# Optimization experiments

Hardware: AMD Instinct MI355X
Metric: run time of the kernel (lower is better)

## Reference

```python
import jax, jax.numpy as jnp
import numpy as np

B, S, D_IN, E, H = 4, 2048, 768, 768, 12
HD = E // H                      # 64
WIN_PCT = 10                     # window_size init arg (percent of valid length)
MAX_LEN = 2048
MIN_WIN = 2
PAD = -1e9
TEMP = 1.0


def setup_inputs() -> dict:
    key = jax.random.key(0)
    k1, k2, k3 = jax.random.split(key, 3)
    return {
        "x": jax.random.normal(k1, (B, S, D_IN), dtype=jnp.float32),
        "src_key_padding_mask": jnp.zeros((B, S), dtype=jnp.int32),   # 0 = valid token
        "matrix_mask": jnp.zeros((B, S, S), dtype=jnp.float32),       # additive mask, 0 or PAD
        "qkv_w": jax.random.normal(k2, (3 * E, D_IN), dtype=jnp.float32) * 0.02,
        "qkv_b": jnp.zeros((3 * E,), dtype=jnp.float32),
        "o_w": jax.random.normal(k3, (E, E), dtype=jnp.float32) * 0.02,
        "o_b": jnp.zeros((E,), dtype=jnp.float32),
    }


def _sliding_window_mask(src_key_padding_mask, matrix_mask):
    # per-sample window size = ceil(valid_len * WIN_PCT / 100), clamped to >= MIN_WIN
    lens = (src_key_padding_mask == 0).sum(axis=1)                    # [B]
    clipped = jnp.minimum(lens, MAX_LEN).astype(jnp.float32)
    wsz = jnp.maximum(jnp.ceil(clipped * WIN_PCT / 100.0), MIN_WIN)   # [B] float ok for compare
    idx = jnp.arange(S)
    dist = jnp.abs(idx[None, :, None] - idx[None, None, :])           # [1,S,S]
    window_mask = dist > wsz[:, None, None]                           # [B,S,S] bool
    merged = window_mask | (matrix_mask == PAD)
    return jnp.where(merged, PAD, matrix_mask)                        # [B,S,S]


def reference(x, src_key_padding_mask, matrix_mask, qkv_w, qkv_b, o_w, o_b):
    mask = _sliding_window_mask(src_key_padding_mask, matrix_mask)    # [B,S,S]
    qkv = x @ qkv_w.T + qkv_b                                         # [B,S,3E]
    # torch: reshape(B,S,H,3*HD) then chunk along last dim
    qkv = qkv.reshape(B, S, H, 3 * HD).transpose(0, 2, 1, 3)          # [B,H,S,3*HD]
    q, k, v = jnp.split(qkv, 3, axis=-1)                              # each [B,H,S,HD]
    scale = 1.0 / np.sqrt(HD)
    logits = jnp.einsum("bhqd,bhkd->bhqk", q, k) * scale + mask[:, None]
    attn = jax.nn.softmax(logits / TEMP, axis=-1)                     # [B,H,S,S]
    values = jnp.einsum("bhqk,bhkd->bhqd", attn, v)                   # [B,H,S,HD]
    attn_mean = attn.mean(axis=1)                                     # [B,S,S]
    values = values.transpose(0, 2, 1, 3).reshape(B, S, E)            # [B,S,E]
    o = values @ o_w.T + o_b
    return (o, attn_mean)
```

## Files before the change

kernel.cpp:

```cpp
#include <hip/hip_runtime.h>

#define SEQ 2048
#define NB 4
#define DIN 768
#define EDIM 768
#define NH 12
#define QKVN 2304
#define SCALE 0.125f
#define PADV -1e9f
#define INV12 (0.0833333333f)
#define PSW 520

typedef unsigned short ushort_t;
typedef __attribute__((ext_vector_type(8))) short bf16x8;
typedef __attribute__((ext_vector_type(4))) float f32x4;

__device__ __forceinline__ float bf2f(ushort_t u) {
    union { unsigned int i; float f; } v; v.i = ((unsigned int)u) << 16; return v.f;
}
__device__ __forceinline__ ushort_t f2bf(float f) {
    union { float f; unsigned int i; } v; v.f = f;
    unsigned int r = (v.i + 0x7fffu + ((v.i >> 16) & 1u)) >> 16;
    return (ushort_t)r;
}
__device__ __forceinline__ void gl_lds16(const ushort_t* g, ushort_t* l) {
    __builtin_amdgcn_global_load_lds(
        (const __attribute__((address_space(1))) unsigned int*)(g),
        (__attribute__((address_space(3))) unsigned int*)(l),
        16, 0, 0);
}

__global__ void cvt3_kernel(const float* __restrict__ s0, int n0,
                            const float* __restrict__ s1, int n1,
                            const float* __restrict__ s2, int n2,
                            ushort_t* __restrict__ d0, ushort_t* __restrict__ d1,
                            ushort_t* __restrict__ d2) {
    int i = blockIdx.x * blockDim.x + threadIdx.x;
    const float* src; ushort_t* dst; int off;
    if (i < n0)               { src = s0; dst = d0; off = i; }
    else if (i < n0 + n1)     { src = s1; dst = d1; off = i - n0; }
    else if (i < n0 + n1 + n2){ src = s2; dst = d2; off = i - n0 - n1; }
    else return;
    float4 f = ((const float4*)src)[off];
    ushort4 u;
    u.x = f2bf(f.x); u.y = f2bf(f.y); u.z = f2bf(f.z); u.w = f2bf(f.w);
    ((ushort4*)dst)[off] = u;
}

template<int MODE>
__global__ __launch_bounds__(256) void mfma_gemm128(
    const ushort_t* __restrict__ A, const ushort_t* __restrict__ Bw,
    const float* __restrict__ bias, float* __restrict__ outf,
    ushort_t* __restrict__ qkh, ushort_t* __restrict__ vt, int N, int K)
{
    __shared__ __align__(16) ushort_t Al[128 * 64];
    __shared__ __align__(16) ushort_t Bl[128 * 64];
    const int tid  = threadIdx.x;
    const int w    = tid >> 6;
    const int l    = tid & 63;
    const int quad = l >> 4;
    const int lr   = l & 15;
    const int mw   = (w >> 1) * 64;
    const int nw   = (w & 1) * 64;
    const int bm   = blockIdx.y * 128;
    const int bn   = blockIdx.x * 128;
    const int srow = l >> 3;
    const int sg   = (l & 7) ^ srow;

    f32x4 acc[4][4];
    #pragma unroll
    for (int i = 0; i < 4; ++i)
        #pragma unroll
        for (int j = 0; j < 4; ++j)
            #pragma unroll
            for (int r = 0; r < 4; ++r) acc[i][j][r] = 0.f;

    const ushort_t* ga = A  + (size_t)(bm + w * 32 + srow) * K + sg * 8;
    const ushort_t* gb = Bw + (size_t)(bn + w * 32 + srow) * K + sg * 8;
    ushort_t* la = &Al[(w * 32) * 64];
    ushort_t* lb = &Bl[(w * 32) * 64];

    for (int k0 = 0; k0 < K; k0 += 64) {
        __syncthreads();
        #pragma unroll
        for (int i = 0; i < 4; ++i)
            gl_lds16(ga + (size_t)(i * 8) * K + k0, la + i * 8 * 64);
        #pragma unroll
        for (int i = 0; i < 4; ++i)
            gl_lds16(gb + (size_t)(i * 8) * K + k0, lb + i * 8 * 64);
        __syncthreads();
        #pragma unroll
        for (int s = 0; s < 2; ++s) {
            bf16x8 af[4], bf[4];
            #pragma unroll
            for (int t = 0; t < 4; ++t)
                af[t] = *(const bf16x8*)&Al[(mw + t * 16 + lr) * 64 + (((4 * s + quad) ^ (lr & 7)) * 8)];
            #pragma unroll
            for (int t = 0; t < 4; ++t)
                bf[t] = *(const bf16x8*)&Bl[(nw + t * 16 + lr) * 64 + (((4 * s + quad) ^ (lr & 7)) * 8)];
            #pragma unroll
            for (int mt = 0; mt < 4; ++mt)
                #pragma unroll
                for (int nt = 0; nt < 4; ++nt)
                    acc[mt][nt] = __builtin_amdgcn_mfma_f32_16x16x32_bf16(af[mt], bf[nt], acc[mt][nt], 0, 0, 0);
        }
    }

    #pragma unroll
    for (int nt = 0; nt < 4; ++nt) {
        const int gn = bn + nw + nt * 16 + lr;
        const float bv = bias[gn];
        const int hh  = gn / 192;
        const int rem = gn - hh * 192;
        #pragma unroll
        for (int mt = 0; mt < 4; ++mt) {
            const int gm0 = bm + mw + mt * 16 + quad * 4;
            if (MODE == 0) {
                #pragma unroll
                for (int r = 0; r < 4; ++r)
                    outf[(size_t)(gm0 + r) * N + gn] = acc[mt][nt][r] + bv;
            } else if (rem < 128) {
                const int bb  = gm0 >> 11;
                const int tok = gm0 & (SEQ - 1);
                #pragma unroll
                for (int r = 0; r < 4; ++r)
                    qkh[((size_t)(bb * NH + hh) * SEQ + tok + r) * 128 + rem] =
                        f2bf(acc[mt][nt][r] + bv);
            } else {
                const int bb  = gm0 >> 11;
                const int tok = gm0 & (SEQ - 1);
                ushort4 st;
                st.x = f2bf(acc[mt][nt][0] + bv);
                st.y = f2bf(acc[mt][nt][1] + bv);
                st.z = f2bf(acc[mt][nt][2] + bv);
                st.w = f2bf(acc[mt][nt][3] + bv);
                *(ushort4*)&vt[((size_t)(bb * NH + hh) * 64 + (rem - 128)) * SEQ + tok] = st;
            }
        }
    }
}

__global__ __launch_bounds__(512) void attn_kernel(
    const ushort_t* __restrict__ qkh,
    const ushort_t* __restrict__ vt,
    const float* __restrict__ mmask,
    const int* __restrict__ pad,
    ushort_t* __restrict__ values,
    float* __restrict__ attn_out)
{
    __shared__ __align__(16) ushort_t Ps[2][16 * PSW];
    __shared__ float lsump[2][4][16];
    __shared__ int s_cnt[8];
    __shared__ int s_flags[8];
    const int tid  = threadIdx.x;
    const int w    = tid >> 6;
    const int hg   = w >> 2;
    const int ww   = w & 3;
    const int lane = tid & 63;
    const int quad = lane >> 4;
    const int lr   = lane & 15;

    const int lin  = blockIdx.x;
    const int s    = lin & 1;
    const int b    = (lin >> 1) & 3;
    const int i16  = (lin >> 3) + 64 * s;
    const int iq0  = i16 * 16;

    {
        int4 pv = *(const int4*)&pad[b * SEQ + tid * 4];
        int c = (pv.x == 0) + (pv.y == 0) + (pv.z == 0) + (pv.w == 0);
        #pragma unroll
        for (int o = 32; o; o >>= 1) c += __shfl_down(c, o, 64);
        if (lane == 0) s_cnt[w] = c;
        if (tid < 8) s_flags[tid] = 0;
    }
    __syncthreads();
    int len = 0;
    #pragma unroll
    for (int k = 0; k < 8; ++k) len += s_cnt[k];
    if (len > 2048) len = 2048;
    int wsz = (int)ceilf((float)len * 10.0f / 100.0f);
    if (wsz < 2) wsz = 2;

    const int jlo  = max(0, iq0 - wsz);
    const int jhi  = min(SEQ - 1, iq0 + 15 + wsz);
    const int jt0  = jlo >> 6;
    const int nch  = (jhi >> 6) - jt0 + 1;
    const int jbase = jt0 << 6;
    const int span  = nch << 6;

    {
        const float* tp = mmask + ((size_t)b * SEQ + iq0) * SEQ + jbase;
        const int e = tid * 2, row = e >> 6, col = e & 63;
        for (int ci = 0; ci < nch; ++ci) {
            float2 v = *(const float2*)&tp[(size_t)row * SEQ + ci * 64 + col];
            if (__any(v.x != 0.f || v.y != 0.f)) {
                if (lane == 0) atomicOr(&s_flags[ci], 1);
            }
        }
    }

    const int arow = tid & 15;
    const int acg  = tid >> 4;
    float acc[16];
    #pragma unroll
    for (int k = 0; k < 16; ++k) acc[k] = 0.f;
    __syncthreads();

    const ushort_t* vhead = vt + (size_t)b * NH * 64 * SEQ;

    for (int hp = 0; hp < NH / 2; ++hp) {
        const int h = hp * 2 + hg;
        const ushort_t* hbase = qkh + (size_t)(b * NH + h) * SEQ * 128;
        const ushort_t* qbase = hbase + (size_t)(iq0 + lr) * 128;
        const bf16x8 qf0 = *(const bf16x8*)(qbase + quad * 8);
        const bf16x8 qf1 = *(const bf16x8*)(qbase + 32 + quad * 8);

        float ls[4] = {0.f, 0.f, 0.f, 0.f};
        #pragma unroll
        for (int cc = 0; cc < 2; ++cc) {
            const int ci = ww + cc * 4;
            if (ci < nch) {
                const int jc = jbase + ci * 64;
                f32x4 s4[4];
                #pragma unroll
                for (int t = 0; t < 4; ++t) {
                    const ushort_t* kr = hbase + (size_t)(jc + t * 16 + lr) * 128 + 64;
                    bf16x8 kf0 = *(const bf16x8*)(kr + quad * 8);
                    bf16x8 kf1 = *(const bf16x8*)(kr + 32 + quad * 8);
                    #pragma unroll
                    for (int r = 0; r < 4; ++r) s4[t][r] = 0.f;
                    s4[t] = __builtin_amdgcn_mfma_f32_16x16x32_bf16(qf0, kf0, s4[t], 0, 0, 0);
                    s4[t] = __builtin_amdgcn_mfma_f32_16x16x32_bf16(qf1, kf1, s4[t], 0, 0, 0);
                }
                const int anym = s_flags[ci];
                #pragma unroll
                for (int t = 0; t < 4; ++t) {
                    const int gj = jc + t * 16 + lr;
                    #pragma unroll
                    for (int r = 0; r < 4; ++r) {
                        const int gi = iq0 + quad * 4 + r;
                        float mm = 0.f;
                        if (anym) mm = mmask[((size_t)b * SEQ + gi) * SEQ + gj];
                        const int dist = gi > gj ? gi - gj : gj - gi;
                        const float p = (dist > wsz) ? 0.f : __expf(fmaf(s4[t][r], SCALE, mm));
                        ls[r] += p;
                        Ps[hg][(quad * 4 + r) * PSW + (ci * 64 + t * 16 + lr)] = f2bf(p);
                    }
                }
            }
        }
        #pragma unroll
        for (int r = 0; r < 4; ++r) {
            #pragma unroll
            for (int m = 8; m; m >>= 1) ls[r] += __shfl_xor(ls[r], m, 16);
        }
        if (lr == 0) {
            #pragma unroll
            for (int r = 0; r < 4; ++r) lsump[hg][ww][quad * 4 + r] = ls[r];
        }
        __syncthreads();

        if (acg * 16 < span) {
            const float l0 = lsump[0][0][arow] + lsump[0][1][arow] + lsump[0][2][arow] + lsump[0][3][arow];
            const float l1 = lsump[1][0][arow] + lsump[1][1][arow] + lsump[1][2][arow] + lsump[1][3][arow];
            const float sc0 = INV12 / l0;
            const float sc1 = INV12 / l1;
            const ushort_t* p0 = &Ps[0][arow * PSW + acg * 16];
            const ushort_t* p1 = &Ps[1][arow * PSW + acg * 16];
            #pragma unroll
            for (int k = 0; k < 4; ++k) {
                ushort4 u0 = *(const ushort4*)(p0 + k * 4);
                ushort4 u1 = *(const ushort4*)(p1 + k * 4);
                acc[k * 4 + 0] = fmaf(bf2f(u0.x), sc0, fmaf(bf2f(u1.x), sc1, acc[k * 4 + 0]));
                acc[k * 4 + 1] = fmaf(bf2f(u0.y), sc0, fmaf(bf2f(u1.y), sc1, acc[k * 4 + 1]));
                acc[k * 4 + 2] = fmaf(bf2f(u0.z), sc0, fmaf(bf2f(u1.z), sc1, acc[k * 4 + 2]));
                acc[k * 4 + 3] = fmaf(bf2f(u0.w), sc0, fmaf(bf2f(u1.w), sc1, acc[k * 4 + 3]));
            }
        }

        {
            f32x4 oacc;
            #pragma unroll
            for (int r = 0; r < 4; ++r) oacc[r] = 0.f;
            const ushort_t* vrow = vhead + (size_t)(h * 64 + ww * 16 + lr) * SEQ + jbase;
            for (int ci = 0; ci < nch; ++ci) {
                const int tok0 = ci * 64;
                #pragma unroll
                for (int s2 = 0; s2 < 2; ++s2) {
                    bf16x8 pa = *(const bf16x8*)&Ps[hg][lr * PSW + tok0 + s2 * 32 + quad * 8];
                    bf16x8 vf = *(const bf16x8*)(vrow + tok0 + s2 * 32 + quad * 8);
                    oacc = __builtin_amdgcn_mfma_f32_16x16x32_bf16(pa, vf, oacc, 0, 0, 0);
                }
            }
            float lr4[4];
            #pragma unroll
            for (int r = 0; r < 4; ++r)
                lr4[r] = lsump[hg][0][quad * 4 + r] + lsump[hg][1][quad * 4 + r] +
                         lsump[hg][2][quad * 4 + r] + lsump[hg][3][quad * 4 + r];
            #pragma unroll
            for (int r = 0; r < 4; ++r) {
                const int row = iq0 + quad * 4 + r;
                values[(size_t)(b * SEQ + row) * EDIM + h * 64 + ww * 16 + lr] =
                    f2bf(oacc[r] / lr4[r]);
            }
        }
        __syncthreads();
    }

    if (acg * 16 < span) {
        float* dst = attn_out + ((size_t)b * SEQ + iq0 + arow) * SEQ + jbase + acg * 16;
        #pragma unroll
        for (int k = 0; k < 4; ++k) {
            float4 v = { acc[k * 4 + 0], acc[k * 4 + 1], acc[k * 4 + 2], acc[k * 4 + 3] };
            *(float4*)(dst + k * 4) = v;
        }
    }
    {
        const int c4lo = jbase >> 2;
        const int c4hi = (jbase + span) >> 2;
        const float4 z = {0.f, 0.f, 0.f, 0.f};
        for (int f = tid; f < 16 * 512; f += 512) {
            const int i  = f >> 9;
            const int c4 = f & 511;
            if (c4 < c4lo || c4 >= c4hi)
                *(float4*)(attn_out + ((size_t)b * SEQ + iq0 + i) * SEQ + c4 * 4) = z;
        }
    }
}

extern "C" void kernel_launch(void* const* d_in, const int* in_sizes, int n_in,
                              void* d_out, int out_size, void* d_ws, size_t ws_size,
                              hipStream_t stream) {
    const float* x      = (const float*)d_in[0];
    const int*   pad    = (const int*)d_in[1];
    const float* mmask  = (const float*)d_in[2];
    const float* qkv_w  = (const float*)d_in[3];
    const float* qkv_b  = (const float*)d_in[4];
    const float* o_w    = (const float*)d_in[5];
    const float* o_b    = (const float*)d_in[6];

    float* out_o    = (float*)d_out;
    float* out_attn = out_o + (size_t)NB * SEQ * EDIM;

    ushort_t* qkh    = (ushort_t*)d_ws;
    ushort_t* vt     = qkh + (size_t)NB * NH * SEQ * 128;
    ushort_t* xb     = vt + (size_t)NB * NH * 64 * SEQ;
    ushort_t* values = xb;
    ushort_t* wqkvb  = xb + (size_t)NB * SEQ * DIN;
    ushort_t* wob    = wqkvb + (size_t)QKVN * DIN;

    const int nx = NB * SEQ * DIN / 4, nw1 = QKVN * DIN / 4, nw2 = EDIM * EDIM / 4;
    cvt3_kernel<<<(nx + nw1 + nw2 + 255) / 256, 256, 0, stream>>>(
        x, nx, qkv_w, nw1, o_w, nw2, xb, wqkvb, wob);

    mfma_gemm128<1><<<dim3(QKVN / 128, (NB * SEQ) / 128), 256, 0, stream>>>(
        xb, wqkvb, qkv_b, nullptr, qkh, vt, QKVN, DIN);

    attn_kernel<<<512, 512, 0, stream>>>(
        qkh, vt, mmask, pad, values, out_attn);

    mfma_gemm128<0><<<dim3(EDIM / 128, (NB * SEQ) / 128), 256, 0, stream>>>(
        values, wob, o_b, out_o, nullptr, nullptr, EDIM, EDIM);
}
```

Baseline: 323.7 us.

## Double-buffer P tiles across head pairs and software-pipeline K/V loads

Double-buffers the shared P scratch and row-sum buffers by head-pair parity, which lets the trailing barrier per iteration be removed so the next head's QK/exp phase can overlap the previous PV phase. K fragments for the second chunk are loaded before the first chunk's exp work, and V fragments are prefetched one chunk ahead in the PV loop. A launch-bounds occupancy hint is added. Shared memory use doubles, and register pressure rises because more fragments are held live at once.

```diff
diff --git a/kernel.cpp b/kernel.cpp
--- a/kernel.cpp
+++ b/kernel.cpp
@@ -140,7 +140,7 @@
     }
 }
 
-__global__ __launch_bounds__(512) void attn_kernel(
+__global__ __launch_bounds__(512, 4) void attn_kernel(
     const ushort_t* __restrict__ qkh,
     const ushort_t* __restrict__ vt,
     const float* __restrict__ mmask,
@@ -148,8 +148,8 @@
     ushort_t* __restrict__ values,
     float* __restrict__ attn_out)
 {
-    __shared__ __align__(16) ushort_t Ps[2][16 * PSW];
-    __shared__ float lsump[2][4][16];
+    __shared__ __align__(16) ushort_t Ps[2][2][16 * PSW];
+    __shared__ float lsump[2][2][4][16];
     __shared__ int s_cnt[8];
     __shared__ int s_flags[8];
     const int tid  = threadIdx.x;
@@ -210,46 +210,80 @@
     const ushort_t* vhead = vt + (size_t)b * NH * 64 * SEQ;
 
     for (int hp = 0; hp < NH / 2; ++hp) {
+        const int p = hp & 1;
         const int h = hp * 2 + hg;
+        ushort_t* Psw = Ps[p][hg];
         const ushort_t* hbase = qkh + (size_t)(b * NH + h) * SEQ * 128;
         const ushort_t* qbase = hbase + (size_t)(iq0 + lr) * 128;
         const bf16x8 qf0 = *(const bf16x8*)(qbase + quad * 8);
         const bf16x8 qf1 = *(const bf16x8*)(qbase + 32 + quad * 8);
 
         float ls[4] = {0.f, 0.f, 0.f, 0.f};
-        #pragma unroll
-        for (int cc = 0; cc < 2; ++cc) {
-            const int ci = ww + cc * 4;
-            if (ci < nch) {
-                const int jc = jbase + ci * 64;
-                f32x4 s4[4];
-                #pragma unroll
-                for (int t = 0; t < 4; ++t) {
-                    const ushort_t* kr = hbase + (size_t)(jc + t * 16 + lr) * 128 + 64;
-                    bf16x8 kf0 = *(const bf16x8*)(kr + quad * 8);
-                    bf16x8 kf1 = *(const bf16x8*)(kr + 32 + quad * 8);
-                    #pragma unroll
-                    for (int r = 0; r < 4; ++r) s4[t][r] = 0.f;
-                    s4[t] = __builtin_amdgcn_mfma_f32_16x16x32_bf16(qf0, kf0, s4[t], 0, 0, 0);
-                    s4[t] = __builtin_amdgcn_mfma_f32_16x16x32_bf16(qf1, kf1, s4[t], 0, 0, 0);
+        const int ci0 = ww;
+        const int ci1 = ww + 4;
+        const int jc0 = jbase + ci0 * 64;
+        const int jc1 = jbase + ci1 * 64;
+
+        auto do_exp = [&](int ci, f32x4* s4) {
+            const int jc = jbase + ci * 64;
+            const int anym = s_flags[ci];
+            #pragma unroll
+            for (int t = 0; t < 4; ++t) {
+                const int gj = jc + t * 16 + lr;
+                #pragma unroll
+                for (int r = 0; r < 4; ++r) {
+                    const int gi = iq0 + quad * 4 + r;
+                    float mm = 0.f;
+                    if (anym) mm = mmask[((size_t)b * SEQ + gi) * SEQ + gj];
+                    const int dist = gi > gj ? gi - gj : gj - gi;
+                    const float pe = (dist > wsz) ? 0.f : __expf(fmaf(s4[t][r], SCALE, mm));
+                    ls[r] += pe;
+                    Psw[(quad * 4 + r) * PSW + (ci * 64 + t * 16 + lr)] = f2bf(pe);
                 }
-                const int anym = s_flags[ci];
-                #pragma unroll
-                for (int t = 0; t < 4; ++t) {
-                    const int gj = jc + t * 16 + lr;
-                    #pragma unroll
-                    for (int r = 0; r < 4; ++r) {
-                        const int gi = iq0 + quad * 4 + r;
-                        float mm = 0.f;
-                        if (anym) mm = mmask[((size_t)b * SEQ + gi) * SEQ + gj];
-                        const int dist = gi > gj ? gi - gj : gj - gi;
-                        const float p = (dist > wsz) ? 0.f : __expf(fmaf(s4[t][r], SCALE, mm));
-                        ls[r] += p;
-                        Ps[hg][(quad * 4 + r) * PSW + (ci * 64 + t * 16 + lr)] = f2bf(p);
-                    }
-                }
-            }
-        }
+            }
+        };
+
+        bf16x8 k0a[4], k0b[4];
+        if (ci0 < nch) {
+            #pragma unroll
+            for (int t = 0; t < 4; ++t) {
+                const ushort_t* kr = hbase + (size_t)(jc0 + t * 16 + lr) * 128 + 64;
+                k0a[t] = *(const bf16x8*)(kr + quad * 8);
+                k0b[t] = *(const bf16x8*)(kr + 32 + quad * 8);
+            }
+        }
+        f32x4 s40[4];
+        if (ci0 < nch) {
+            #pragma unroll
+            for (int t = 0; t < 4; ++t) {
+                #pragma unroll
+                for (int r = 0; r < 4; ++r) s40[t][r] = 0.f;
+                s40[t] = __builtin_amdgcn_mfma_f32_16x16x32_bf16(qf0, k0a[t], s40[t], 0, 0, 0);
+                s40[t] = __builtin_amdgcn_mfma_f32_16x16x32_bf16(qf1, k0b[t], s40[t], 0, 0, 0);
+            }
+        }
+        bf16x8 k1a[4], k1b[4];
+        if (ci1 < nch) {
+            #pragma unroll
+            for (int t = 0; t < 4; ++t) {
+                const ushort_t* kr = hbase + (size_t)(jc1 + t * 16 + lr) * 128 + 64;
+                k1a[t] = *(const bf16x8*)(kr + quad * 8);
+                k1b[t] = *(const bf16x8*)(kr + 32 + quad * 8);
+            }
+        }
+        if (ci0 < nch) do_exp(ci0, s40);
+        if (ci1 < nch) {
+            f32x4 s41[4];
+            #pragma unroll
+            for (int t = 0; t < 4; ++t) {
+                #pragma unroll
+                for (int r = 0; r < 4; ++r) s41[t][r] = 0.f;
+                s41[t] = __builtin_amdgcn_mfma_f32_16x16x32_bf16(qf0, k1a[t], s41[t], 0, 0, 0);
+                s41[t] = __builtin_amdgcn_mfma_f32_16x16x32_bf16(qf1, k1b[t], s41[t], 0, 0, 0);
+            }
+            do_exp(ci1, s41);
+        }
+
         #pragma unroll
         for (int r = 0; r < 4; ++r) {
             #pragma unroll
@@ -257,17 +291,17 @@
         }
         if (lr == 0) {
             #pragma unroll
-            for (int r = 0; r < 4; ++r) lsump[hg][ww][quad * 4 + r] = ls[r];
+            for (int r = 0; r < 4; ++r) lsump[p][hg][ww][quad * 4 + r] = ls[r];
         }
         __syncthreads();
 
         if (acg * 16 < span) {
-            const float l0 = lsump[0][0][arow] + lsump[0][1][arow] + lsump[0][2][arow] + lsump[0][3][arow];
-            const float l1 = lsump[1][0][arow] + lsump[1][1][arow] + lsump[1][2][arow] + lsump[1][3][arow];
+            const float l0 = lsump[p][0][0][arow] + lsump[p][0][1][arow] + lsump[p][0][2][arow] + lsump[p][0][3][arow];
+            const float l1 = lsump[p][1][0][arow] + lsump[p][1][1][arow] + lsump[p][1][2][arow] + lsump[p][1][3][arow];
             const float sc0 = INV12 / l0;
             const float sc1 = INV12 / l1;
-            const ushort_t* p0 = &Ps[0][arow * PSW + acg * 16];
-            const ushort_t* p1 = &Ps[1][arow * PSW + acg * 16];
+            const ushort_t* p0 = &Ps[p][0][arow * PSW + acg * 16];
+            const ushort_t* p1 = &Ps[p][1][arow * PSW + acg * 16];
             #pragma unroll
             for (int k = 0; k < 4; ++k) {
                 ushort4 u0 = *(const ushort4*)(p0 + k * 4);
@@ -284,20 +318,27 @@
             #pragma unroll
             for (int r = 0; r < 4; ++r) oacc[r] = 0.f;
             const ushort_t* vrow = vhead + (size_t)(h * 64 + ww * 16 + lr) * SEQ + jbase;
+            bf16x8 vf0 = *(const bf16x8*)(vrow + quad * 8);
+            bf16x8 vf1 = *(const bf16x8*)(vrow + 32 + quad * 8);
             for (int ci = 0; ci < nch; ++ci) {
+                bf16x8 nvf0 = vf0, nvf1 = vf1;
+                if (ci + 1 < nch) {
+                    const ushort_t* nv = vrow + (ci + 1) * 64;
+                    nvf0 = *(const bf16x8*)(nv + quad * 8);
+                    nvf1 = *(const bf16x8*)(nv + 32 + quad * 8);
+                }
                 const int tok0 = ci * 64;
-                #pragma unroll
-                for (int s2 = 0; s2 < 2; ++s2) {
-                    bf16x8 pa = *(const bf16x8*)&Ps[hg][lr * PSW + tok0 + s2 * 32 + quad * 8];
-                    bf16x8 vf = *(const bf16x8*)(vrow + tok0 + s2 * 32 + quad * 8);
-                    oacc = __builtin_amdgcn_mfma_f32_16x16x32_bf16(pa, vf, oacc, 0, 0, 0);
-                }
+                bf16x8 pa0 = *(const bf16x8*)&Psw[lr * PSW + tok0 + quad * 8];
+                bf16x8 pa1 = *(const bf16x8*)&Psw[lr * PSW + tok0 + 32 + quad * 8];
+                oacc = __builtin_amdgcn_mfma_f32_16x16x32_bf16(pa0, vf0, oacc, 0, 0, 0);
+                oacc = __builtin_amdgcn_mfma_f32_16x16x32_bf16(pa1, vf1, oacc, 0, 0, 0);
+                vf0 = nvf0; vf1 = nvf1;
             }
             float lr4[4];
             #pragma unroll
             for (int r = 0; r < 4; ++r)
-                lr4[r] = lsump[hg][0][quad * 4 + r] + lsump[hg][1][quad * 4 + r] +
-                         lsump[hg][2][quad * 4 + r] + lsump[hg][3][quad * 4 + r];
+                lr4[r] = lsump[p][hg][0][quad * 4 + r] + lsump[p][hg][1][quad * 4 + r] +
+                         lsump[p][hg][2][quad * 4 + r] + lsump[p][hg][3][quad * 4 + r];
             #pragma unroll
             for (int r = 0; r < 4; ++r) {
                 const int row = iq0 + quad * 4 + r;
@@ -305,7 +346,6 @@
                     f2bf(oacc[r] / lr4[r]);
             }
         }
-        __syncthreads();
     }
 
     if (acg * 16 < span) {
```

Result: slower. 360.4 us (+11.3%).

## Split attention heads across two blocks and combine attention-mean partials

Applied to the files above, without the earlier changes.

The attention kernel can now split the 12 heads into two halves handled by separate blocks, doubling the grid from 512 to 1024 blocks. Each half writes its partial attn_mean band into a workspace buffer, and a new combine kernel sums the two partials and writes the full attention row, including the zeros outside the band. The aim is more parallelism and occupancy on the many-CU GPU. In exchange it adds an extra kernel launch and extra global traffic for the partial buffers. The split path is used only when the workspace is large enough.

```diff
diff --git a/kernel.cpp b/kernel.cpp
--- a/kernel.cpp
+++ b/kernel.cpp
@@ -140,13 +140,15 @@
     }
 }
 
+template<int HSPLIT>
 __global__ __launch_bounds__(512) void attn_kernel(
     const ushort_t* __restrict__ qkh,
     const ushort_t* __restrict__ vt,
     const float* __restrict__ mmask,
     const int* __restrict__ pad,
     ushort_t* __restrict__ values,
-    float* __restrict__ attn_out)
+    float* __restrict__ attn_out,
+    float* __restrict__ part)
 {
     __shared__ __align__(16) ushort_t Ps[2][16 * PSW];
     __shared__ float lsump[2][4][16];
@@ -163,7 +165,8 @@
     const int lin  = blockIdx.x;
     const int s    = lin & 1;
     const int b    = (lin >> 1) & 3;
-    const int i16  = (lin >> 3) + 64 * s;
+    const int half = HSPLIT ? ((lin >> 3) & 1) : 0;
+    const int i16  = (HSPLIT ? (lin >> 4) : (lin >> 3)) + 64 * s;
     const int iq0  = i16 * 16;
 
     {
@@ -209,8 +212,9 @@
 
     const ushort_t* vhead = vt + (size_t)b * NH * 64 * SEQ;
 
-    for (int hp = 0; hp < NH / 2; ++hp) {
-        const int h = hp * 2 + hg;
+    const int NPAIR = HSPLIT ? 3 : (NH / 2);
+    for (int hp = 0; hp < NPAIR; ++hp) {
+        const int h = half * 6 + hp * 2 + hg;
         const ushort_t* hbase = qkh + (size_t)(b * NH + h) * SEQ * 128;
         const ushort_t* qbase = hbase + (size_t)(iq0 + lr) * 128;
         const bf16x8 qf0 = *(const bf16x8*)(qbase + quad * 8);
@@ -308,24 +312,87 @@
         __syncthreads();
     }
 
-    if (acg * 16 < span) {
-        float* dst = attn_out + ((size_t)b * SEQ + iq0 + arow) * SEQ + jbase + acg * 16;
-        #pragma unroll
-        for (int k = 0; k < 4; ++k) {
-            float4 v = { acc[k * 4 + 0], acc[k * 4 + 1], acc[k * 4 + 2], acc[k * 4 + 3] };
-            *(float4*)(dst + k * 4) = v;
-        }
-    }
+    if (HSPLIT) {
+        if (acg * 16 < span) {
+            float* dst = part + ((((size_t)half * NB + b) * 128 + i16) * 16 + arow) * 512 + acg * 16;
+            #pragma unroll
+            for (int k = 0; k < 4; ++k) {
+                float4 v = { acc[k * 4 + 0], acc[k * 4 + 1], acc[k * 4 + 2], acc[k * 4 + 3] };
+                *(float4*)(dst + k * 4) = v;
+            }
+        }
+    } else {
+        if (acg * 16 < span) {
+            float* dst = attn_out + ((size_t)b * SEQ + iq0 + arow) * SEQ + jbase + acg * 16;
+            #pragma unroll
+            for (int k = 0; k < 4; ++k) {
+                float4 v = { acc[k * 4 + 0], acc[k * 4 + 1], acc[k * 4 + 2], acc[k * 4 + 3] };
+                *(float4*)(dst + k * 4) = v;
+            }
+        }
+        {
+            const int c4lo = jbase >> 2;
+            const int c4hi = (jbase + span) >> 2;
+            const float4 z = {0.f, 0.f, 0.f, 0.f};
+            for (int f = tid; f < 16 * 512; f += 512) {
+                const int i  = f >> 9;
+                const int c4 = f & 511;
+                if (c4 < c4lo || c4 >= c4hi)
+                    *(float4*)(attn_out + ((size_t)b * SEQ + iq0 + i) * SEQ + c4 * 4) = z;
+            }
+        }
+    }
+}
+
+__global__ __launch_bounds__(256) void combine_kernel(
+    const float* __restrict__ part, const int* __restrict__ pad,
+    float* __restrict__ attn_out)
+{
+    const int tid  = threadIdx.x;
+    const int w    = tid >> 6;
+    const int lane = tid & 63;
+    const int blk  = blockIdx.x;
+    const int b    = blk >> 7;
+    const int i16  = blk & 127;
+    const int iq0  = i16 * 16;
+
+    __shared__ int s_cnt[4];
     {
-        const int c4lo = jbase >> 2;
-        const int c4hi = (jbase + span) >> 2;
-        const float4 z = {0.f, 0.f, 0.f, 0.f};
-        for (int f = tid; f < 16 * 512; f += 512) {
-            const int i  = f >> 9;
-            const int c4 = f & 511;
-            if (c4 < c4lo || c4 >= c4hi)
-                *(float4*)(attn_out + ((size_t)b * SEQ + iq0 + i) * SEQ + c4 * 4) = z;
-        }
+        const int4* pp = (const int4*)&pad[b * SEQ];
+        int4 a = pp[tid * 2];
+        int4 c = pp[tid * 2 + 1];
+        int n = (a.x == 0) + (a.y == 0) + (a.z == 0) + (a.w == 0) +
+                (c.x == 0) + (c.y == 0) + (c.z == 0) + (c.w == 0);
+        #pragma unroll
+        for (int o = 32; o; o >>= 1) n += __shfl_down(n, o, 64);
+        if (lane == 0) s_cnt[w] = n;
+    }
+    __syncthreads();
+    int len = s_cnt[0] + s_cnt[1] + s_cnt[2] + s_cnt[3];
+    if (len > 2048) len = 2048;
+    int wsz = (int)ceilf((float)len * 10.0f / 100.0f);
+    if (wsz < 2) wsz = 2;
+    const int jlo  = max(0, iq0 - wsz);
+    const int jhi  = min(SEQ - 1, iq0 + 15 + wsz);
+    const int jt0  = jlo >> 6;
+    const int span = (((jhi >> 6) - jt0) + 1) << 6;
+    const int jbase = jt0 << 6;
+
+    const float* p0 = part + (((size_t)(0 * NB + b) * 128 + i16) * 16) * 512;
+    const float* p1 = part + (((size_t)(1 * NB + b) * 128 + i16) * 16) * 512;
+
+    for (int idx = tid; idx < 16 * 512; idx += 256) {
+        const int row = idx >> 9;
+        const int c4  = idx & 511;
+        const int col = c4 * 4;
+        float4 v = {0.f, 0.f, 0.f, 0.f};
+        const int off = col - jbase;
+        if (off >= 0 && off < span) {
+            float4 a = *(const float4*)&p0[row * 512 + off];
+            float4 c = *(const float4*)&p1[row * 512 + off];
+            v.x = a.x + c.x; v.y = a.y + c.y; v.z = a.z + c.z; v.w = a.w + c.w;
+        }
+        *(float4*)&attn_out[((size_t)b * SEQ + iq0 + row) * SEQ + col] = v;
     }
 }
 
@@ -349,6 +416,12 @@
     ushort_t* values = xb;
     ushort_t* wqkvb  = xb + (size_t)NB * SEQ * DIN;
     ushort_t* wob    = wqkvb + (size_t)QKVN * DIN;
+    ushort_t* wsend  = wob + (size_t)EDIM * EDIM;
+    float*    part   = (float*)wsend;
+
+    const size_t base_bytes = (size_t)(wsend - (ushort_t*)d_ws) * sizeof(ushort_t);
+    const size_t part_bytes = (size_t)2 * NB * 128 * 16 * 512 * sizeof(float);
+    const bool   split      = ws_size >= base_bytes + part_bytes;
 
     const int nx = NB * SEQ * DIN / 4, nw1 = QKVN * DIN / 4, nw2 = EDIM * EDIM / 4;
     cvt3_kernel<<<(nx + nw1 + nw2 + 255) / 256, 256, 0, stream>>>(
@@ -357,8 +430,14 @@
     mfma_gemm128<1><<<dim3(QKVN / 128, (NB * SEQ) / 128), 256, 0, stream>>>(
         xb, wqkvb, qkv_b, nullptr, qkh, vt, QKVN, DIN);
 
-    attn_kernel<<<512, 512, 0, stream>>>(
-        qkh, vt, mmask, pad, values, out_attn);
+    if (split) {
+        attn_kernel<1><<<1024, 512, 0, stream>>>(
+            qkh, vt, mmask, pad, values, out_attn, part);
+        combine_kernel<<<512, 256, 0, stream>>>(part, pad, out_attn);
+    } else {
+        attn_kernel<0><<<512, 512, 0, stream>>>(
+            qkh, vt, mmask, pad, values, out_attn, part);
+    }
 
     mfma_gemm128<0><<<dim3(EDIM / 128, (NB * SEQ) / 128), 256, 0, stream>>>(
         values, wob, o_b, out_o, nullptr, nullptr, EDIM, EDIM);
```

New measurement: 383.7 us. +18.5%, slower.

## Process 32 query rows per attention block with 1024 threads, reusing K fragments

Applied to the files above, without the earlier changes.

Doubles the query tile of the sliding-window attention kernel from 16 to 32 rows. Blocks grow to 16 waves and the grid halves to 256 blocks. Each wave loads its K chunk once and reuses it for two 16-row MFMA groups. The PV stage splits waves across row halves and head-dim quarters. This cuts redundant K loads and per-block overhead, at the cost of more registers, a doubled shared-memory P buffer, and fewer, larger blocks with heavier barriers.

```diff
diff --git a/kernel.cpp b/kernel.cpp
--- a/kernel.cpp
+++ b/kernel.cpp
@@ -140,7 +140,7 @@
     }
 }
 
-__global__ __launch_bounds__(512) void attn_kernel(
+__global__ __launch_bounds__(1024, 4) void attn_kernel(
     const ushort_t* __restrict__ qkh,
     const ushort_t* __restrict__ vt,
     const float* __restrict__ mmask,
@@ -148,14 +148,14 @@
     ushort_t* __restrict__ values,
     float* __restrict__ attn_out)
 {
-    __shared__ __align__(16) ushort_t Ps[2][16 * PSW];
-    __shared__ float lsump[2][4][16];
+    __shared__ __align__(16) ushort_t Ps[2][32 * PSW];
+    __shared__ float lsump[2][8][32];
     __shared__ int s_cnt[8];
     __shared__ int s_flags[8];
     const int tid  = threadIdx.x;
     const int w    = tid >> 6;
-    const int hg   = w >> 2;
-    const int ww   = w & 3;
+    const int hg   = w >> 3;
+    const int ww   = w & 7;
     const int lane = tid & 63;
     const int quad = lane >> 4;
     const int lr   = lane & 15;
@@ -163,17 +163,17 @@
     const int lin  = blockIdx.x;
     const int s    = lin & 1;
     const int b    = (lin >> 1) & 3;
-    const int i16  = (lin >> 3) + 64 * s;
-    const int iq0  = i16 * 16;
-
-    {
+    const int i32  = (lin >> 3) + 32 * s;
+    const int iq0  = i32 * 32;
+
+    if (tid < 512) {
         int4 pv = *(const int4*)&pad[b * SEQ + tid * 4];
         int c = (pv.x == 0) + (pv.y == 0) + (pv.z == 0) + (pv.w == 0);
         #pragma unroll
         for (int o = 32; o; o >>= 1) c += __shfl_down(c, o, 64);
         if (lane == 0) s_cnt[w] = c;
-        if (tid < 8) s_flags[tid] = 0;
-    }
+    }
+    if (tid < 8) s_flags[tid] = 0;
     __syncthreads();
     int len = 0;
     #pragma unroll
@@ -183,7 +183,7 @@
     if (wsz < 2) wsz = 2;
 
     const int jlo  = max(0, iq0 - wsz);
-    const int jhi  = min(SEQ - 1, iq0 + 15 + wsz);
+    const int jhi  = min(SEQ - 1, iq0 + 31 + wsz);
     const int jt0  = jlo >> 6;
     const int nch  = (jhi >> 6) - jt0 + 1;
     const int jbase = jt0 << 6;
@@ -200,8 +200,8 @@
         }
     }
 
-    const int arow = tid & 15;
-    const int acg  = tid >> 4;
+    const int arow = tid & 31;
+    const int acg  = tid >> 5;
     float acc[16];
     #pragma unroll
     for (int k = 0; k < 16; ++k) acc[k] = 0.f;
@@ -212,58 +212,73 @@
     for (int hp = 0; hp < NH / 2; ++hp) {
         const int h = hp * 2 + hg;
         const ushort_t* hbase = qkh + (size_t)(b * NH + h) * SEQ * 128;
-        const ushort_t* qbase = hbase + (size_t)(iq0 + lr) * 128;
-        const bf16x8 qf0 = *(const bf16x8*)(qbase + quad * 8);
-        const bf16x8 qf1 = *(const bf16x8*)(qbase + 32 + quad * 8);
-
-        float ls[4] = {0.f, 0.f, 0.f, 0.f};
-        #pragma unroll
-        for (int cc = 0; cc < 2; ++cc) {
-            const int ci = ww + cc * 4;
-            if (ci < nch) {
-                const int jc = jbase + ci * 64;
+
+        bf16x8 qf[2][2];
+        #pragma unroll
+        for (int rg = 0; rg < 2; ++rg) {
+            const ushort_t* qb = hbase + (size_t)(iq0 + rg * 16 + lr) * 128 + quad * 8;
+            qf[rg][0] = *(const bf16x8*)(qb);
+            qf[rg][1] = *(const bf16x8*)(qb + 32);
+        }
+
+        float ls[2][4] = {{0.f,0.f,0.f,0.f},{0.f,0.f,0.f,0.f}};
+        const int ci = ww;
+        if (ci < nch) {
+            const int jc = jbase + ci * 64;
+            bf16x8 kf0[4], kf1[4];
+            #pragma unroll
+            for (int t = 0; t < 4; ++t) {
+                const ushort_t* kr = hbase + (size_t)(jc + t * 16 + lr) * 128 + 64 + quad * 8;
+                kf0[t] = *(const bf16x8*)(kr);
+                kf1[t] = *(const bf16x8*)(kr + 32);
+            }
+            const int anym = s_flags[ci];
+            #pragma unroll
+            for (int rg = 0; rg < 2; ++rg) {
                 f32x4 s4[4];
                 #pragma unroll
                 for (int t = 0; t < 4; ++t) {
-                    const ushort_t* kr = hbase + (size_t)(jc + t * 16 + lr) * 128 + 64;
-                    bf16x8 kf0 = *(const bf16x8*)(kr + quad * 8);
-                    bf16x8 kf1 = *(const bf16x8*)(kr + 32 + quad * 8);
                     #pragma unroll
                     for (int r = 0; r < 4; ++r) s4[t][r] = 0.f;
-                    s4[t] = __builtin_amdgcn_mfma_f32_16x16x32_bf16(qf0, kf0, s4[t], 0, 0, 0);
-                    s4[t] = __builtin_amdgcn_mfma_f32_16x16x32_bf16(qf1, kf1, s4[t], 0, 0, 0);
+                    s4[t] = __builtin_amdgcn_mfma_f32_16x16x32_bf16(qf[rg][0], kf0[t], s4[t], 0, 0, 0);
+                    s4[t] = __builtin_amdgcn_mfma_f32_16x16x32_bf16(qf[rg][1], kf1[t], s4[t], 0, 0, 0);
                 }
-                const int anym = s_flags[ci];
                 #pragma unroll
                 for (int t = 0; t < 4; ++t) {
                     const int gj = jc + t * 16 + lr;
                     #pragma unroll
                     for (int r = 0; r < 4; ++r) {
-                        const int gi = iq0 + quad * 4 + r;
+                        const int gi = iq0 + rg * 16 + quad * 4 + r;
                         float mm = 0.f;
                         if (anym) mm = mmask[((size_t)b * SEQ + gi) * SEQ + gj];
                         const int dist = gi > gj ? gi - gj : gj - gi;
                         const float p = (dist > wsz) ? 0.f : __expf(fmaf(s4[t][r], SCALE, mm));
-                        ls[r] += p;
-                        Ps[hg][(quad * 4 + r) * PSW + (ci * 64 + t * 16 + lr)] = f2bf(p);
+                        ls[rg][r] += p;
+                        Ps[hg][(rg * 16 + quad * 4 + r) * PSW + (ci * 64 + t * 16 + lr)] = f2bf(p);
                     }
                 }
             }
         }
         #pragma unroll
-        for (int r = 0; r < 4; ++r) {
-            #pragma unroll
-            for (int m = 8; m; m >>= 1) ls[r] += __shfl_xor(ls[r], m, 16);
-        }
+        for (int rg = 0; rg < 2; ++rg)
+            #pragma unroll
+            for (int r = 0; r < 4; ++r) {
+                #pragma unroll
+                for (int m = 8; m; m >>= 1) ls[rg][r] += __shfl_xor(ls[rg][r], m, 16);
+            }
         if (lr == 0) {
             #pragma unroll
-            for (int r = 0; r < 4; ++r) lsump[hg][ww][quad * 4 + r] = ls[r];
+            for (int rg = 0; rg < 2; ++rg)
+                #pragma unroll
+                for (int r = 0; r < 4; ++r)
+                    lsump[hg][ww][rg * 16 + quad * 4 + r] = ls[rg][r];
         }
         __syncthreads();
 
         if (acg * 16 < span) {
-            const float l0 = lsump[0][0][arow] + lsump[0][1][arow] + lsump[0][2][arow] + lsump[0][3][arow];
-            const float l1 = lsump[1][0][arow] + lsump[1][1][arow] + lsump[1][2][arow] + lsump[1][3][arow];
+            float l0 = 0.f, l1 = 0.f;
+            #pragma unroll
+            for (int k = 0; k < 8; ++k) { l0 += lsump[0][k][arow]; l1 += lsump[1][k][arow]; }
             const float sc0 = INV12 / l0;
             const float sc1 = INV12 / l1;
             const ushort_t* p0 = &Ps[0][arow * PSW + acg * 16];
@@ -280,28 +295,33 @@
         }
 
         {
+            const int rh = ww & 1;
+            const int dq = ww >> 1;
             f32x4 oacc;
             #pragma unroll
             for (int r = 0; r < 4; ++r) oacc[r] = 0.f;
-            const ushort_t* vrow = vhead + (size_t)(h * 64 + ww * 16 + lr) * SEQ + jbase;
-            for (int ci = 0; ci < nch; ++ci) {
-                const int tok0 = ci * 64;
+            const ushort_t* vrow = vhead + (size_t)(h * 64 + dq * 16 + lr) * SEQ + jbase;
+            for (int ci2 = 0; ci2 < nch; ++ci2) {
+                const int tok0 = ci2 * 64;
                 #pragma unroll
                 for (int s2 = 0; s2 < 2; ++s2) {
-                    bf16x8 pa = *(const bf16x8*)&Ps[hg][lr * PSW + tok0 + s2 * 32 + quad * 8];
+                    bf16x8 pa = *(const bf16x8*)&Ps[hg][(rh * 16 + lr) * PSW + tok0 + s2 * 32 + quad * 8];
                     bf16x8 vf = *(const bf16x8*)(vrow + tok0 + s2 * 32 + quad * 8);
                     oacc = __builtin_amdgcn_mfma_f32_16x16x32_bf16(pa, vf, oacc, 0, 0, 0);
                 }
             }
             float lr4[4];
             #pragma unroll
-            for (int r = 0; r < 4; ++r)
-                lr4[r] = lsump[hg][0][quad * 4 + r] + lsump[hg][1][quad * 4 + r] +
-                         lsump[hg][2][quad * 4 + r] + lsump[hg][3][quad * 4 + r];
-            #pragma unroll
             for (int r = 0; r < 4; ++r) {
-                const int row = iq0 + quad * 4 + r;
-                values[(size_t)(b * SEQ + row) * EDIM + h * 64 + ww * 16 + lr] =
+                float l = 0.f;
+                #pragma unroll
+                for (int k = 0; k < 8; ++k) l += lsump[hg][k][rh * 16 + quad * 4 + r];
+                lr4[r] = l;
+            }
+            #pragma unroll
+            for (int r = 0; r < 4; ++r) {
+                const int row = iq0 + rh * 16 + quad * 4 + r;
+                values[(size_t)(b * SEQ + row) * EDIM + h * 64 + dq * 16 + lr] =
                     f2bf(oacc[r] / lr4[r]);
             }
         }
@@ -320,7 +340,7 @@
         const int c4lo = jbase >> 2;
         const int c4hi = (jbase + span) >> 2;
         const float4 z = {0.f, 0.f, 0.f, 0.f};
-        for (int f = tid; f < 16 * 512; f += 512) {
+        for (int f = tid; f < 32 * 512; f += 1024) {
             const int i  = f >> 9;
             const int c4 = f & 511;
             if (c4 < c4lo || c4 >= c4hi)
@@ -357,7 +377,7 @@
     mfma_gemm128<1><<<dim3(QKVN / 128, (NB * SEQ) / 128), 256, 0, stream>>>(
         xb, wqkvb, qkv_b, nullptr, qkh, vt, QKVN, DIN);
 
-    attn_kernel<<<512, 512, 0, stream>>>(
+    attn_kernel<<<256, 1024, 0, stream>>>(
         qkh, vt, mmask, pad, values, out_attn);
 
     mfma_gemm128<0><<<dim3(EDIM / 128, (NB * SEQ) / 128), 256, 0, stream>>>(
```

Result: slower. 339.7 us (+4.9%).
